# Kernel optimization log

Hardware: AMD Instinct MI355X
Metric: run time of the kernel (lower is better)

## Reference

```python
import jax, jax.numpy as jnp
import numpy as np

EMBED_DIM = 1024
NUM_HEADS = 16
HEAD_DIM = EMBED_DIM // NUM_HEADS


def setup_inputs() -> dict:
    key = jax.random.key(0)
    ks = jax.random.split(key, 11)
    N, S, D = 2, 2048, EMBED_DIM
    scale = 1.0 / np.sqrt(D)
    inp = {
        "query": jax.random.normal(ks[0], (N, S, D), jnp.float32),
        "key": jax.random.normal(ks[1], (N, S, D), jnp.float32),
        "value": jax.random.normal(ks[2], (N, S, D), jnp.float32),
        # Dense layer params (kernel [D_in, D_out], bias [D_out])
        "Wq": jax.random.normal(ks[3], (D, D), jnp.float32) * scale,
        "bq": jnp.zeros((D,), jnp.float32),
        "Wk": jax.random.normal(ks[4], (D, D), jnp.float32) * scale,
        "bk": jnp.zeros((D,), jnp.float32),
        "Wv": jax.random.normal(ks[5], (D, D), jnp.float32) * scale,
        "bv": jnp.zeros((D,), jnp.float32),
        "Wp": jax.random.normal(ks[6], (D, D), jnp.float32) * scale,
        "bp": jnp.zeros((D,), jnp.float32),
    }
    return inp


def reference(query, key, value, Wq, bq, Wk, bk, Wv, bv, Wp, bp):
    N, S, D = query.shape
    H, Hd = NUM_HEADS, D // NUM_HEADS
    # Linear projections, then split heads: [N, H, S, Hd]
    def split_heads(x):
        return x.reshape(N, S, H, Hd).transpose(0, 2, 1, 3)
    q = split_heads(query @ Wq + bq)
    k = split_heads(key @ Wk + bk)
    v = split_heads(value @ Wv + bv)
    # Scaled dot-product attention; materializes [N, H, S, S] scores
    e = jnp.einsum("bhsd,bhtd->bhst", q, k) / jnp.sqrt(jnp.asarray(Hd, jnp.float32))
    a = jax.nn.softmax(e, axis=-1)
    # Dropout is identity in inference mode (keras Dropout default)
    out = jnp.einsum("bhst,bhtd->bhsd", a, v)
    out = out.transpose(0, 2, 1, 3).reshape(N, S, D)
    return out @ Wp + bp
```

## Files before the change

kernel.cpp:

```cpp
#include <hip/hip_runtime.h>
#include <cstdint>
#include <cstddef>

typedef _Float16 f16;
typedef f16 f16x2 __attribute__((ext_vector_type(2)));
typedef f16 f16x8 __attribute__((ext_vector_type(8)));
typedef __fp16 hf16x2 __attribute__((ext_vector_type(2)));
typedef float f32x4 __attribute__((ext_vector_type(4)));
typedef float f32x16 __attribute__((ext_vector_type(16)));
typedef unsigned int u32;

#define S_LEN 2048
#define DIM 1024
#define NBATCH 2
#define NHEAD 16
#define HDIM 64
#define M_TOT (NBATCH * S_LEN)

#define QSCALE 0.18033688011112042f

#define OFF_XQ 0ull
#define OFF_XK (OFF_XQ + (size_t)M_TOT * DIM * 2)
#define OFF_XV (OFF_XK + (size_t)M_TOT * DIM * 2)
#define OFF_WT (OFF_XV + (size_t)M_TOT * DIM * 2)
#define OFF_Q  (OFF_WT + 4ull * DIM * DIM * 2)
#define OFF_K  (OFF_Q + (size_t)M_TOT * DIM * 2)
#define OFF_VT (OFF_K + (size_t)M_TOT * DIM * 2)
#define OFF_AO (OFF_VT + (size_t)M_TOT * DIM * 2)

typedef const __attribute__((address_space(1))) void GVp;
typedef __attribute__((address_space(3))) void LVp;
__device__ __forceinline__ void gload16(const void* g, void* l) {
  __builtin_amdgcn_global_load_lds((GVp*)g, (LVp*)l, 16, 0, 0);
}

__device__ __forceinline__ float fast_exp2(float x) {
  float r;
  asm("v_exp_f32 %0, %1" : "=v"(r) : "v"(x));
  return r;
}

__global__ __launch_bounds__(256) void cast_x_kernel(
    const float* __restrict__ q, const float* __restrict__ k, const float* __restrict__ v,
    f16* __restrict__ oq, f16* __restrict__ ok, f16* __restrict__ ov) {
  const float* src = blockIdx.y == 0 ? q : blockIdx.y == 1 ? k : v;
  f16* dst = blockIdx.y == 0 ? oq : blockIdx.y == 1 ? ok : ov;
  size_t i = ((size_t)blockIdx.x * 256 + threadIdx.x) * 8;
  float4 a = *(const float4*)(src + i);
  float4 b = *(const float4*)(src + i + 4);
  f16x8 o;
  o[0] = (f16)a.x; o[1] = (f16)a.y; o[2] = (f16)a.z; o[3] = (f16)a.w;
  o[4] = (f16)b.x; o[5] = (f16)b.y; o[6] = (f16)b.z; o[7] = (f16)b.w;
  *(f16x8*)(dst + i) = o;
}

__global__ __launch_bounds__(256) void transpose_w_kernel(
    const float* __restrict__ Wq, const float* __restrict__ Wk,
    const float* __restrict__ Wv, const float* __restrict__ Wp,
    f16* __restrict__ out) {
  const float* W = blockIdx.z == 0 ? Wq : blockIdx.z == 1 ? Wk : blockIdx.z == 2 ? Wv : Wp;
  f16* Wt = out + (size_t)blockIdx.z * DIM * DIM;
  __shared__ f16 tile[64][72];
  const int kt = blockIdx.x * 64, nt = blockIdx.y * 64;
  const int t = threadIdx.x, r = t >> 2, c0 = (t & 3) * 16;
#pragma unroll
  for (int i = 0; i < 16; i += 4) {
    float4 vv = *(const float4*)(W + (size_t)(kt + r) * DIM + nt + c0 + i);
    tile[r][c0 + i + 0] = (f16)vv.x; tile[r][c0 + i + 1] = (f16)vv.y;
    tile[r][c0 + i + 2] = (f16)vv.z; tile[r][c0 + i + 3] = (f16)vv.w;
  }
  __syncthreads();
  f16x8 o0, o1;
#pragma unroll
  for (int i = 0; i < 8; ++i) { o0[i] = tile[c0 + i][r]; o1[i] = tile[c0 + 8 + i][r]; }
  *(f16x8*)(Wt + (size_t)(nt + r) * DIM + kt + c0) = o0;
  *(f16x8*)(Wt + (size_t)(nt + r) * DIM + kt + c0 + 8) = o1;
}

__device__ __forceinline__ void gemm_core(const f16* __restrict__ A, const f16* __restrict__ B,
                                          char* lds, f32x4 acc[4][4]) {
  const int tid = threadIdx.x;
  const int wid = tid >> 6, lane = tid & 63;
  const int l15 = lane & 15, l4 = lane >> 4;
  const int wm = (wid >> 1) * 64, wn = (wid & 1) * 64;
  const int srow = tid >> 2;
  const int scol = (tid & 3) * 8;
  const f16* gA = A + (size_t)srow * DIM + scol;
  const f16* gB = B + (size_t)srow * DIM + scol;
  const int ldst = wid * 1024;

  gload16(gA,            lds + ldst);
  gload16(gA + 64 * DIM, lds + 4096 + ldst);
  gload16(gB,            lds + 8192 + ldst);
  gload16(gB + 64 * DIM, lds + 12288 + ldst);
  __syncthreads();

  for (int kt = 0; kt < DIM / 32; ++kt) {
    char* cur = lds + (kt & 1) * 16384;
    if (kt + 1 < DIM / 32) {
      char* nxt = lds + ((kt + 1) & 1) * 16384;
      const f16* ga = gA + (kt + 1) * 32;
      const f16* gb = gB + (kt + 1) * 32;
      gload16(ga,            nxt + ldst);
      gload16(ga + 64 * DIM, nxt + 4096 + ldst);
      gload16(gb,            nxt + 8192 + ldst);
      gload16(gb + 64 * DIM, nxt + 12288 + ldst);
    }
    f16x8 af[4], bf[4];
#pragma unroll
    for (int mt = 0; mt < 4; ++mt)
      af[mt] = *(const f16x8*)(cur + (wm + mt * 16 + l15) * 64 + l4 * 16);
#pragma unroll
    for (int nt = 0; nt < 4; ++nt)
      bf[nt] = *(const f16x8*)(cur + 8192 + (wn + nt * 16 + l15) * 64 + l4 * 16);
#pragma unroll
    for (int mt = 0; mt < 4; ++mt)
#pragma unroll
      for (int nt = 0; nt < 4; ++nt)
        acc[mt][nt] = __builtin_amdgcn_mfma_f32_16x16x32_f16(af[mt], bf[nt], acc[mt][nt], 0, 0, 0);
    __syncthreads();
  }
}


__global__ __launch_bounds__(256) void proj_kernel(
    const f16* __restrict__ Xq, const f16* __restrict__ Xk, const f16* __restrict__ Xv,
    const f16* __restrict__ Wt,
    const float* __restrict__ bq, const float* __restrict__ bk, const float* __restrict__ bv,
    f16* __restrict__ Q, f16* __restrict__ Kh, f16* __restrict__ Vt) {
  __shared__ __align__(16) char lds[32768];
  const int m0 = blockIdx.x * 128, n0 = blockIdx.y * 128;
  const int z = blockIdx.z;
  const f16* X = z == 0 ? Xq : z == 1 ? Xk : Xv;
  const f16* W = Wt + (size_t)z * DIM * DIM;
  const float* bias = z == 0 ? bq : z == 1 ? bk : bv;
  f32x4 acc[4][4] = {};
  gemm_core(X + (size_t)m0 * DIM, W + (size_t)n0 * DIM, lds, acc);

  const int tid = threadIdx.x, wid = tid >> 6, lane = tid & 63;
  const int l15 = lane & 15, l4 = lane >> 4;
  const int wm = (wid >> 1) * 64, wn = (wid & 1) * 64;
#pragma unroll
  for (int nt = 0; nt < 4; ++nt) {
    const int col = n0 + wn + nt * 16 + l15;
    const float bb = bias[col];
    const int hh = col >> 6, d = col & 63;
#pragma unroll
    for (int mt = 0; mt < 4; ++mt)
#pragma unroll
      for (int j = 0; j < 4; ++j) {
        const int row = m0 + wm + mt * 16 + l4 * 4 + j;
        const float v = acc[mt][nt][j] + bb;
        const int n = row >> 11, s = row & (S_LEN - 1);
        const size_t panel = (size_t)(n * NHEAD + hh);
        if (z == 0) {
          const size_t a = panel * (S_LEN * HDIM) + (size_t)(s >> 5) * 2048 +
                           (d >> 4) * 512 + ((d >> 3) & 1) * 256 + (s & 31) * 8 + (d & 7);
          Q[a] = (f16)(v * QSCALE);
        } else if (z == 1) {
          const size_t a = panel * (S_LEN * HDIM) + (size_t)(s >> 5) * 2048 +
                           (d >> 4) * 512 + ((d >> 3) & 1) * 256 + (s & 31) * 8 + (d & 7);
          Kh[a] = (f16)v;
        } else {
          const size_t a = panel * (S_LEN * HDIM) + (size_t)(s >> 6) * 4096 +
                           (d >> 5) * 2048 + ((s >> 4) & 3) * 512 + ((s >> 3) & 1) * 256 +
                           (d & 31) * 8 + (s & 7);
          Vt[a] = (f16)v;
        }
      }
  }
}

__global__ __launch_bounds__(256) void outproj_kernel(
    const f16* __restrict__ A, const f16* __restrict__ Wt,
    const float* __restrict__ bias, float* __restrict__ Out) {
  __shared__ __align__(16) char lds[32768];
  const int m0 = blockIdx.x * 128, n0 = blockIdx.y * 128;
  f32x4 acc[4][4] = {};
  gemm_core(A + (size_t)m0 * DIM, Wt + (size_t)n0 * DIM, lds, acc);

  const int tid = threadIdx.x, wid = tid >> 6, lane = tid & 63;
  const int l15 = lane & 15, l4 = lane >> 4;
  const int wm = (wid >> 1) * 64, wn = (wid & 1) * 64;
#pragma unroll
  for (int nt = 0; nt < 4; ++nt) {
    const int col = n0 + wn + nt * 16 + l15;
    const float bb = bias[col];
#pragma unroll
    for (int mt = 0; mt < 4; ++mt)
#pragma unroll
      for (int j = 0; j < 4; ++j) {
        const int row = m0 + wm + mt * 16 + l4 * 4 + j;
        Out[(size_t)row * DIM + col] = acc[mt][nt][j] + bb;
      }
  }
}

__global__ __launch_bounds__(256, 1) void attn_kernel(
    const f16* __restrict__ Q, const f16* __restrict__ K,
    const f16* __restrict__ Vt, f16* __restrict__ AO) {
  const int qt = blockIdx.x, h = blockIdx.y, b = blockIdx.z;
  const int lane = threadIdx.x & 63, wid = threadIdx.x >> 6;
  const int l31 = lane & 31, hi = lane >> 5;

  const int q0 = qt * 128 + wid * 32;
  const size_t panel = (size_t)(b * NHEAD + h) * (S_LEN * HDIM);
  const f16* Qp = Q + panel + (size_t)(q0 >> 5) * 2048;
  const f16* Kp = K + panel;
  const f16* Vp = Vt + panel;

  f16x8 qf[4];
#pragma unroll
  for (int sk = 0; sk < 4; ++sk)
    qf[sk] = *(const f16x8*)(Qp + sk * 512 + hi * 256 + l31 * 8);

  f32x16 accO[2] = {};
  float lacc0 = 0.f, lacc1 = 0.f, lacc2 = 0.f, lacc3 = 0.f;

  auto LOADK = [&](int it, f16x8 (&kf)[2][4]) {
#pragma unroll
    for (int tt = 0; tt < 2; ++tt)
#pragma unroll
      for (int sk = 0; sk < 4; ++sk)
        kf[tt][sk] = *(const f16x8*)(Kp + (size_t)(it * 2 + tt) * 2048 + sk * 512 + hi * 256 + l31 * 8);
  };
  auto LOADV = [&](int it, f16x8 (&vf)[2][4]) {
#pragma unroll
    for (int dt = 0; dt < 2; ++dt)
#pragma unroll
      for (int s = 0; s < 4; ++s)
        vf[dt][s] = *(const f16x8*)(Vp + (size_t)it * 4096 + dt * 2048 + s * 512 + hi * 256 + l31 * 8);
  };
  auto QK = [&](const f16x8 (&kf)[2][4], f32x16 (&st)[2]) {
    __builtin_amdgcn_s_setprio(1);
#pragma unroll
    for (int tt = 0; tt < 2; ++tt) {
      st[tt] = (f32x16)(0.f);
#pragma unroll
      for (int sk = 0; sk < 4; ++sk)
        st[tt] = __builtin_amdgcn_mfma_f32_32x32x16_f16(kf[tt][sk], qf[sk], st[tt], 0, 0, 0);
    }
    __builtin_amdgcn_s_setprio(0);
  };

  auto PHASE = [&](f32x16 (&st)[2], const f16x8 (&vf)[2][4]) {
    u32 pk[2][8];
#pragma unroll
    for (int tt = 0; tt < 2; ++tt)
#pragma unroll
      for (int j = 0; j < 8; ++j) {
        const float p0 = fast_exp2(st[tt][2 * j]);
        const float p1 = fast_exp2(st[tt][2 * j + 1]);
        const float ps = p0 + p1;
        if (((tt * 8 + j) & 3) == 0) lacc0 += ps;
        else if (((tt * 8 + j) & 3) == 1) lacc1 += ps;
        else if (((tt * 8 + j) & 3) == 2) lacc2 += ps;
        else lacc3 += ps;
        union { hf16x2 h; u32 w; } cv;
        cv.h = __builtin_amdgcn_cvt_pkrtz(p0, p1);
        pk[tt][j] = cv.w;
      }

    __builtin_amdgcn_s_setprio(1);
#pragma unroll
    for (int s = 0; s < 4; ++s) {
      const int tt = s >> 1, sl = s & 1;
      u32 w0 = pk[tt][4 * sl + 0], w2 = pk[tt][4 * sl + 2];
      u32 w1 = pk[tt][4 * sl + 1], w3 = pk[tt][4 * sl + 3];
      asm("v_permlane32_swap_b32 %0, %1" : "+v"(w0), "+v"(w2));
      asm("v_permlane32_swap_b32 %0, %1" : "+v"(w1), "+v"(w3));
      union { u32 w[4]; f16x8 v; } pf;
      pf.w[0] = w0; pf.w[1] = w1; pf.w[2] = w2; pf.w[3] = w3;
      accO[0] = __builtin_amdgcn_mfma_f32_32x32x16_f16(vf[0][s], pf.v, accO[0], 0, 0, 0);
      accO[1] = __builtin_amdgcn_mfma_f32_32x32x16_f16(vf[1][s], pf.v, accO[1], 0, 0, 0);
    }
    __builtin_amdgcn_s_setprio(0);
  };

  f16x8 kfA[2][4], kfB[2][4], vfA[2][4], vfB[2][4];
  f32x16 st[2];
  LOADK(0, kfA); LOADV(0, vfA);
  LOADK(1, kfB); LOADV(1, vfB);
  QK(kfA, st);

  for (int it = 0; it < S_LEN / 64 - 2; it += 2) {
    PHASE(st, vfA);
    LOADV(it + 2, vfA);
    QK(kfB, st);
    LOADK(it + 2, kfA);
    PHASE(st, vfB);
    LOADV(it + 3, vfB);
    QK(kfA, st);
    LOADK(it + 3, kfB);
  }
  PHASE(st, vfA);
  QK(kfB, st);
  PHASE(st, vfB);

  const float l_loc = (lacc0 + lacc1) + (lacc2 + lacc3);
  const float l_all = l_loc + __shfl_xor(l_loc, 32);
  const float inv = 1.f / l_all;
  f16* aop = AO + ((size_t)(b * S_LEN + q0 + l31)) * DIM + h * HDIM;
#pragma unroll
  for (int dt = 0; dt < 2; ++dt)
#pragma unroll
    for (int j = 0; j < 8; ++j) {
      union { f16x2 h; u32 w; } cv;
      cv.h[0] = (f16)(accO[dt][2 * j] * inv);
      cv.h[1] = (f16)(accO[dt][2 * j + 1] * inv);
      const int d = ((2 * j) & 3) + 8 * ((2 * j) >> 2) + 4 * hi + dt * 32;
      *(f16x2*)(aop + d) = cv.h;
    }
}

extern "C" void kernel_launch(void* const* d_in, const int* in_sizes, int n_in,
                              void* d_out, int out_size, void* d_ws, size_t ws_size,
                              hipStream_t stream) {
  (void)in_sizes; (void)n_in; (void)out_size; (void)ws_size;
  const float* q  = (const float*)d_in[0];
  const float* k  = (const float*)d_in[1];
  const float* v  = (const float*)d_in[2];
  const float* Wq = (const float*)d_in[3];
  const float* bq = (const float*)d_in[4];
  const float* Wk = (const float*)d_in[5];
  const float* bk = (const float*)d_in[6];
  const float* Wv = (const float*)d_in[7];
  const float* bv = (const float*)d_in[8];
  const float* Wp = (const float*)d_in[9];
  const float* bp = (const float*)d_in[10];

  char* ws = (char*)d_ws;
  f16* Xq  = (f16*)(ws + OFF_XQ);
  f16* Xk  = (f16*)(ws + OFF_XK);
  f16* Xv  = (f16*)(ws + OFF_XV);
  f16* Wt  = (f16*)(ws + OFF_WT);
  f16* Qs  = (f16*)(ws + OFF_Q);
  f16* Kh  = (f16*)(ws + OFF_K);
  f16* Vts = (f16*)(ws + OFF_VT);
  f16* AO  = (f16*)(ws + OFF_AO);

  cast_x_kernel<<<dim3(2048, 3, 1), 256, 0, stream>>>(q, k, v, Xq, Xk, Xv);
  transpose_w_kernel<<<dim3(16, 16, 4), 256, 0, stream>>>(Wq, Wk, Wv, Wp, Wt);
  proj_kernel<<<dim3(32, 8, 3), 256, 0, stream>>>(Xq, Xk, Xv, Wt, bq, bk, bv, Qs, Kh, Vts);
  attn_kernel<<<dim3(16, 16, 2), 256, 0, stream>>>(Qs, Kh, Vts, AO);
  outproj_kernel<<<dim3(32, 8, 1), 256, 0, stream>>>(AO, Wt + 3ull * DIM * DIM, bp, (float*)d_out);
}
```

Before: 136.3 us.

## Stage K/V tiles through double-buffered LDS shared across waves in attention

Replaces the per-wave direct global loads of K and V fragments, which had each of the four waves load the same tiles separately, with cooperative block-wide loads into a double-buffered LDS staging area. Each wave then reads its fragments from LDS. The aim is to cut redundant global/L2 traffic by a factor of four and to free the registers that held two sets of prefetched fragments, so launch bounds is raised to allow two blocks per CU. In exchange it adds a __syncthreads per iteration and LDS read latency, and it drops the explicit two-deep register prefetch interleaving.

```diff
diff --git a/kernel.cpp b/kernel.cpp
--- a/kernel.cpp
+++ b/kernel.cpp
@@ -196,18 +196,21 @@
   }
 }
 
-__global__ __launch_bounds__(256, 1) void attn_kernel(
+__global__ __launch_bounds__(256, 2) void attn_kernel(
     const f16* __restrict__ Q, const f16* __restrict__ K,
     const f16* __restrict__ Vt, f16* __restrict__ AO) {
   const int qt = blockIdx.x, h = blockIdx.y, b = blockIdx.z;
-  const int lane = threadIdx.x & 63, wid = threadIdx.x >> 6;
+  const int tid = threadIdx.x;
+  const int lane = tid & 63, wid = tid >> 6;
   const int l31 = lane & 31, hi = lane >> 5;
+
+  __shared__ __align__(16) char kv_lds[2][16384];
 
   const int q0 = qt * 128 + wid * 32;
   const size_t panel = (size_t)(b * NHEAD + h) * (S_LEN * HDIM);
   const f16* Qp = Q + panel + (size_t)(q0 >> 5) * 2048;
-  const f16* Kp = K + panel;
-  const f16* Vp = Vt + panel;
+  const char* KpB = (const char*)(K + panel);
+  const char* VpB = (const char*)(Vt + panel);
 
   f16x8 qf[4];
 #pragma unroll
@@ -217,21 +220,24 @@
   f32x16 accO[2] = {};
   float lacc0 = 0.f, lacc1 = 0.f, lacc2 = 0.f, lacc3 = 0.f;
 
-  auto LOADK = [&](int it, f16x8 (&kf)[2][4]) {
+  auto STAGE = [&](int it, int buf) {
+    const char* gK = KpB + (size_t)it * 8192 + tid * 16;
+    const char* gV = VpB + (size_t)it * 8192 + tid * 16;
+    char* lb = kv_lds[buf] + (tid >> 6) * 1024;
+    gload16(gK,        lb);
+    gload16(gK + 4096, lb + 4096);
+    gload16(gV,        lb + 8192);
+    gload16(gV + 4096, lb + 12288);
+  };
+
+  auto QK = [&](int buf, f32x16 (&st)[2]) {
+    const char* lk = kv_lds[buf];
+    f16x8 kf[2][4];
 #pragma unroll
     for (int tt = 0; tt < 2; ++tt)
 #pragma unroll
       for (int sk = 0; sk < 4; ++sk)
-        kf[tt][sk] = *(const f16x8*)(Kp + (size_t)(it * 2 + tt) * 2048 + sk * 512 + hi * 256 + l31 * 8);
-  };
-  auto LOADV = [&](int it, f16x8 (&vf)[2][4]) {
-#pragma unroll
-    for (int dt = 0; dt < 2; ++dt)
-#pragma unroll
-      for (int s = 0; s < 4; ++s)
-        vf[dt][s] = *(const f16x8*)(Vp + (size_t)it * 4096 + dt * 2048 + s * 512 + hi * 256 + l31 * 8);
-  };
-  auto QK = [&](const f16x8 (&kf)[2][4], f32x16 (&st)[2]) {
+        kf[tt][sk] = *(const f16x8*)(lk + tt * 4096 + sk * 1024 + lane * 16);
     __builtin_amdgcn_s_setprio(1);
 #pragma unroll
     for (int tt = 0; tt < 2; ++tt) {
@@ -243,7 +249,15 @@
     __builtin_amdgcn_s_setprio(0);
   };
 
-  auto PHASE = [&](f32x16 (&st)[2], const f16x8 (&vf)[2][4]) {
+  auto PHASE = [&](f32x16 (&st)[2], int buf) {
+    const char* lv = kv_lds[buf] + 8192;
+    f16x8 vf[2][4];
+#pragma unroll
+    for (int dt = 0; dt < 2; ++dt)
+#pragma unroll
+      for (int s = 0; s < 4; ++s)
+        vf[dt][s] = *(const f16x8*)(lv + dt * 4096 + s * 1024 + lane * 16);
+
     u32 pk[2][8];
 #pragma unroll
     for (int tt = 0; tt < 2; ++tt)
@@ -277,25 +291,18 @@
     __builtin_amdgcn_s_setprio(0);
   };
 
-  f16x8 kfA[2][4], kfB[2][4], vfA[2][4], vfB[2][4];
+  const int NIT = S_LEN / 64;
+  STAGE(0, 0);
+  __syncthreads();
+
   f32x16 st[2];
-  LOADK(0, kfA); LOADV(0, vfA);
-  LOADK(1, kfB); LOADV(1, vfB);
-  QK(kfA, st);
-
-  for (int it = 0; it < S_LEN / 64 - 2; it += 2) {
-    PHASE(st, vfA);
-    LOADV(it + 2, vfA);
-    QK(kfB, st);
-    LOADK(it + 2, kfA);
-    PHASE(st, vfB);
-    LOADV(it + 3, vfB);
-    QK(kfA, st);
-    LOADK(it + 3, kfB);
-  }
-  PHASE(st, vfA);
-  QK(kfB, st);
-  PHASE(st, vfB);
+  for (int it = 0; it < NIT; ++it) {
+    const int buf = it & 1;
+    if (it + 1 < NIT) STAGE(it + 1, buf ^ 1);
+    QK(buf, st);
+    PHASE(st, buf);
+    __syncthreads();
+  }
 
   const float l_loc = (lacc0 + lacc1) + (lacc2 + lacc3);
   const float l_all = l_loc + __shfl_xor(l_loc, 32);
```

Measured after the change: 131.8 us. -3.3%, faster.

## Fuse input fp32 cast into projection GEMM and split attention KV range across waves

Applied to the files above, without the earlier changes.

Drops the separate cast kernel: the projection GEMM now streams fp32 activations straight into LDS and converts them to fp16 while building fragments, which removes one full write-and-reread of the three input tensors. The attention kernel is restructured so each 128-thread block handles 32 queries with two waves, each wave covering half the key sequence. The two partial results are then merged through shared memory. This gives four times as many, smaller blocks, trading higher occupancy and parallelism for extra LDS traffic, a larger A-tile in LDS, and a combine step. The split merge skips max rescaling, which is only valid if the softmax does not subtract a running max.

```diff
diff --git a/kernel.cpp b/kernel.cpp
--- a/kernel.cpp
+++ b/kernel.cpp
@@ -19,10 +19,7 @@
 
 #define QSCALE 0.18033688011112042f
 
-#define OFF_XQ 0ull
-#define OFF_XK (OFF_XQ + (size_t)M_TOT * DIM * 2)
-#define OFF_XV (OFF_XK + (size_t)M_TOT * DIM * 2)
-#define OFF_WT (OFF_XV + (size_t)M_TOT * DIM * 2)
+#define OFF_WT 0ull
 #define OFF_Q  (OFF_WT + 4ull * DIM * DIM * 2)
 #define OFF_K  (OFF_Q + (size_t)M_TOT * DIM * 2)
 #define OFF_VT (OFF_K + (size_t)M_TOT * DIM * 2)
@@ -38,20 +35,6 @@
   float r;
   asm("v_exp_f32 %0, %1" : "=v"(r) : "v"(x));
   return r;
-}
-
-__global__ __launch_bounds__(256) void cast_x_kernel(
-    const float* __restrict__ q, const float* __restrict__ k, const float* __restrict__ v,
-    f16* __restrict__ oq, f16* __restrict__ ok, f16* __restrict__ ov) {
-  const float* src = blockIdx.y == 0 ? q : blockIdx.y == 1 ? k : v;
-  f16* dst = blockIdx.y == 0 ? oq : blockIdx.y == 1 ? ok : ov;
-  size_t i = ((size_t)blockIdx.x * 256 + threadIdx.x) * 8;
-  float4 a = *(const float4*)(src + i);
-  float4 b = *(const float4*)(src + i + 4);
-  f16x8 o;
-  o[0] = (f16)a.x; o[1] = (f16)a.y; o[2] = (f16)a.z; o[3] = (f16)a.w;
-  o[4] = (f16)b.x; o[5] = (f16)b.y; o[6] = (f16)b.z; o[7] = (f16)b.w;
-  *(f16x8*)(dst + i) = o;
 }
 
 __global__ __launch_bounds__(256) void transpose_w_kernel(
@@ -75,6 +58,57 @@
   for (int i = 0; i < 8; ++i) { o0[i] = tile[c0 + i][r]; o1[i] = tile[c0 + 8 + i][r]; }
   *(f16x8*)(Wt + (size_t)(nt + r) * DIM + kt + c0) = o0;
   *(f16x8*)(Wt + (size_t)(nt + r) * DIM + kt + c0 + 8) = o1;
+}
+
+__device__ __forceinline__ void gemm_core_af32(const float* __restrict__ A, const f16* __restrict__ B,
+                                               char* lds, f32x4 acc[4][4]) {
+  const int tid = threadIdx.x;
+  const int wid = tid >> 6, lane = tid & 63;
+  const int l15 = lane & 15, l4 = lane >> 4;
+  const int wm = (wid >> 1) * 64, wn = (wid & 1) * 64;
+  const float* gA = A + (size_t)(tid >> 3) * DIM + (tid & 7) * 4;
+  const f16* gB = B + (size_t)(tid >> 2) * DIM + (tid & 3) * 8;
+  const int ldst = wid * 1024;
+
+  auto stage = [&](int kt, char* buf) {
+    const float* ga = gA + kt * 32;
+    const f16* gb = gB + kt * 32;
+#pragma unroll
+    for (int i = 0; i < 4; ++i)
+      gload16(ga + (size_t)i * 32 * DIM, buf + i * 4096 + ldst);
+    gload16(gb,            buf + 16384 + ldst);
+    gload16(gb + 64 * DIM, buf + 20480 + ldst);
+  };
+
+  stage(0, lds);
+  __syncthreads();
+
+  for (int kt = 0; kt < DIM / 32; ++kt) {
+    char* cur = lds + (kt & 1) * 24576;
+    if (kt + 1 < DIM / 32) stage(kt + 1, lds + ((kt + 1) & 1) * 24576);
+    f16x8 af[4], bf[4];
+#pragma unroll
+    for (int mt = 0; mt < 4; ++mt) {
+      const char* ap = cur + ((wm >> 5) + (mt >> 1)) * 4096 + (((mt & 1) * 16 + l15) * 128) + l4 * 32;
+      f32x4 lo = *(const f32x4*)ap;
+      f32x4 hi = *(const f32x4*)(ap + 16);
+      union { hf16x2 h[4]; f16x8 v; } cv;
+      cv.h[0] = __builtin_amdgcn_cvt_pkrtz(lo[0], lo[1]);
+      cv.h[1] = __builtin_amdgcn_cvt_pkrtz(lo[2], lo[3]);
+      cv.h[2] = __builtin_amdgcn_cvt_pkrtz(hi[0], hi[1]);
+      cv.h[3] = __builtin_amdgcn_cvt_pkrtz(hi[2], hi[3]);
+      af[mt] = cv.v;
+    }
+#pragma unroll
+    for (int nt = 0; nt < 4; ++nt)
+      bf[nt] = *(const f16x8*)(cur + 16384 + (wn + nt * 16 + l15) * 64 + l4 * 16);
+#pragma unroll
+    for (int mt = 0; mt < 4; ++mt)
+#pragma unroll
+      for (int nt = 0; nt < 4; ++nt)
+        acc[mt][nt] = __builtin_amdgcn_mfma_f32_16x16x32_f16(af[mt], bf[nt], acc[mt][nt], 0, 0, 0);
+    __syncthreads();
+  }
 }
 
 __device__ __forceinline__ void gemm_core(const f16* __restrict__ A, const f16* __restrict__ B,
@@ -124,18 +158,18 @@
 
 
 __global__ __launch_bounds__(256) void proj_kernel(
-    const f16* __restrict__ Xq, const f16* __restrict__ Xk, const f16* __restrict__ Xv,
+    const float* __restrict__ Xq, const float* __restrict__ Xk, const float* __restrict__ Xv,
     const f16* __restrict__ Wt,
     const float* __restrict__ bq, const float* __restrict__ bk, const float* __restrict__ bv,
     f16* __restrict__ Q, f16* __restrict__ Kh, f16* __restrict__ Vt) {
-  __shared__ __align__(16) char lds[32768];
+  __shared__ __align__(16) char lds[49152];
   const int m0 = blockIdx.x * 128, n0 = blockIdx.y * 128;
   const int z = blockIdx.z;
-  const f16* X = z == 0 ? Xq : z == 1 ? Xk : Xv;
+  const float* X = z == 0 ? Xq : z == 1 ? Xk : Xv;
   const f16* W = Wt + (size_t)z * DIM * DIM;
   const float* bias = z == 0 ? bq : z == 1 ? bk : bv;
   f32x4 acc[4][4] = {};
-  gemm_core(X + (size_t)m0 * DIM, W + (size_t)n0 * DIM, lds, acc);
+  gemm_core_af32(X + (size_t)m0 * DIM, W + (size_t)n0 * DIM, lds, acc);
 
   const int tid = threadIdx.x, wid = tid >> 6, lane = tid & 63;
   const int l15 = lane & 15, l4 = lane >> 4;
@@ -196,14 +230,17 @@
   }
 }
 
-__global__ __launch_bounds__(256, 1) void attn_kernel(
+__global__ __launch_bounds__(128) void attn_kernel(
     const f16* __restrict__ Q, const f16* __restrict__ K,
     const f16* __restrict__ Vt, f16* __restrict__ AO) {
   const int qt = blockIdx.x, h = blockIdx.y, b = blockIdx.z;
-  const int lane = threadIdx.x & 63, wid = threadIdx.x >> 6;
+  const int tid = threadIdx.x;
+  const int lane = tid & 63, half = tid >> 6;
   const int l31 = lane & 31, hi = lane >> 5;
 
-  const int q0 = qt * 128 + wid * 32;
+  __shared__ float comb[2048 + 64];
+
+  const int q0 = qt * 32;
   const size_t panel = (size_t)(b * NHEAD + h) * (S_LEN * HDIM);
   const f16* Qp = Q + panel + (size_t)(q0 >> 5) * 2048;
   const f16* Kp = K + panel;
@@ -277,13 +314,15 @@
     __builtin_amdgcn_s_setprio(0);
   };
 
+  const int i0 = half * 16;
+
   f16x8 kfA[2][4], kfB[2][4], vfA[2][4], vfB[2][4];
   f32x16 st[2];
-  LOADK(0, kfA); LOADV(0, vfA);
-  LOADK(1, kfB); LOADV(1, vfB);
+  LOADK(i0, kfA); LOADV(i0, vfA);
+  LOADK(i0 + 1, kfB); LOADV(i0 + 1, vfB);
   QK(kfA, st);
 
-  for (int it = 0; it < S_LEN / 64 - 2; it += 2) {
+  for (int it = i0; it < i0 + 14; it += 2) {
     PHASE(st, vfA);
     LOADV(it + 2, vfA);
     QK(kfB, st);
@@ -298,19 +337,36 @@
   PHASE(st, vfB);
 
   const float l_loc = (lacc0 + lacc1) + (lacc2 + lacc3);
-  const float l_all = l_loc + __shfl_xor(l_loc, 32);
-  const float inv = 1.f / l_all;
-  f16* aop = AO + ((size_t)(b * S_LEN + q0 + l31)) * DIM + h * HDIM;
-#pragma unroll
-  for (int dt = 0; dt < 2; ++dt)
-#pragma unroll
-    for (int j = 0; j < 8; ++j) {
-      union { f16x2 h; u32 w; } cv;
-      cv.h[0] = (f16)(accO[dt][2 * j] * inv);
-      cv.h[1] = (f16)(accO[dt][2 * j + 1] * inv);
-      const int d = ((2 * j) & 3) + 8 * ((2 * j) >> 2) + 4 * hi + dt * 32;
-      *(f16x2*)(aop + d) = cv.h;
-    }
+  if (half == 1) {
+#pragma unroll
+    for (int dt = 0; dt < 2; ++dt)
+#pragma unroll
+      for (int j = 0; j < 16; ++j)
+        comb[(dt * 16 + j) * 64 + lane] = accO[dt][j];
+    comb[2048 + lane] = l_loc;
+  }
+  __syncthreads();
+  if (half == 0) {
+#pragma unroll
+    for (int dt = 0; dt < 2; ++dt)
+#pragma unroll
+      for (int j = 0; j < 16; ++j)
+        accO[dt][j] += comb[(dt * 16 + j) * 64 + lane];
+    const float l2 = l_loc + comb[2048 + lane];
+    const float l_all = l2 + __shfl_xor(l2, 32);
+    const float inv = 1.f / l_all;
+    f16* aop = AO + ((size_t)(b * S_LEN + q0 + l31)) * DIM + h * HDIM;
+#pragma unroll
+    for (int dt = 0; dt < 2; ++dt)
+#pragma unroll
+      for (int j = 0; j < 8; ++j) {
+        union { f16x2 h; u32 w; } cv;
+        cv.h[0] = (f16)(accO[dt][2 * j] * inv);
+        cv.h[1] = (f16)(accO[dt][2 * j + 1] * inv);
+        const int d = ((2 * j) & 3) + 8 * ((2 * j) >> 2) + 4 * hi + dt * 32;
+        *(f16x2*)(aop + d) = cv.h;
+      }
+  }
 }
 
 extern "C" void kernel_launch(void* const* d_in, const int* in_sizes, int n_in,
@@ -330,18 +386,14 @@
   const float* bp = (const float*)d_in[10];
 
   char* ws = (char*)d_ws;
-  f16* Xq  = (f16*)(ws + OFF_XQ);
-  f16* Xk  = (f16*)(ws + OFF_XK);
-  f16* Xv  = (f16*)(ws + OFF_XV);
   f16* Wt  = (f16*)(ws + OFF_WT);
   f16* Qs  = (f16*)(ws + OFF_Q);
   f16* Kh  = (f16*)(ws + OFF_K);
   f16* Vts = (f16*)(ws + OFF_VT);
   f16* AO  = (f16*)(ws + OFF_AO);
 
-  cast_x_kernel<<<dim3(2048, 3, 1), 256, 0, stream>>>(q, k, v, Xq, Xk, Xv);
   transpose_w_kernel<<<dim3(16, 16, 4), 256, 0, stream>>>(Wq, Wk, Wv, Wp, Wt);
-  proj_kernel<<<dim3(32, 8, 3), 256, 0, stream>>>(Xq, Xk, Xv, Wt, bq, bk, bv, Qs, Kh, Vts);
-  attn_kernel<<<dim3(16, 16, 2), 256, 0, stream>>>(Qs, Kh, Vts, AO);
+  proj_kernel<<<dim3(32, 8, 3), 256, 0, stream>>>(q, k, v, Wt, bq, bk, bv, Qs, Kh, Vts);
+  attn_kernel<<<dim3(64, 16, 2), 128, 0, stream>>>(Qs, Kh, Vts, AO);
   outproj_kernel<<<dim3(32, 8, 1), 256, 0, stream>>>(AO, Wt + 3ull * DIM * DIM, bp, (float*)d_out);
 }
```

Measured after the change: 135.7 us. No clear change (-0.5%).

## Split attention KV range across two waves and swizzle out-projection LDS

Applied to the files above, without the earlier changes.

The attention kernel now uses 128-thread blocks with one 32-row query tile each. The two waves split the key/value sequence in half and merge their partial outputs and row sums through shared memory. This creates four times as many blocks for better occupancy and latency hiding, at the cost of an LDS reduction. It appears to rely on softmax without a running max, as the original did. Separately, the out-projection GEMM gets an XOR-swizzled LDS layout to reduce bank conflicts.

```diff
diff --git a/kernel.cpp b/kernel.cpp
--- a/kernel.cpp
+++ b/kernel.cpp
@@ -113,6 +113,52 @@
 #pragma unroll
     for (int nt = 0; nt < 4; ++nt)
       bf[nt] = *(const f16x8*)(cur + 8192 + (wn + nt * 16 + l15) * 64 + l4 * 16);
+#pragma unroll
+    for (int mt = 0; mt < 4; ++mt)
+#pragma unroll
+      for (int nt = 0; nt < 4; ++nt)
+        acc[mt][nt] = __builtin_amdgcn_mfma_f32_16x16x32_f16(af[mt], bf[nt], acc[mt][nt], 0, 0, 0);
+    __syncthreads();
+  }
+}
+
+__device__ __forceinline__ void gemm_core_sw(const f16* __restrict__ A, const f16* __restrict__ B,
+                                             char* lds, f32x4 acc[4][4]) {
+  const int tid = threadIdx.x;
+  const int wid = tid >> 6, lane = tid & 63;
+  const int l15 = lane & 15, l4 = lane >> 4;
+  const int wm = (wid >> 1) * 64, wn = (wid & 1) * 64;
+  const int rr = tid >> 2, cc = tid & 3;
+  const int ccs = cc ^ ((rr >> 1) & 3);
+  const f16* gA = A + (size_t)rr * DIM + ccs * 8;
+  const f16* gB = B + (size_t)rr * DIM + ccs * 8;
+  const int ldst = wid * 1024;
+
+  gload16(gA,            lds + ldst);
+  gload16(gA + 64 * DIM, lds + 4096 + ldst);
+  gload16(gB,            lds + 8192 + ldst);
+  gload16(gB + 64 * DIM, lds + 12288 + ldst);
+  __syncthreads();
+
+  const int sw = (l15 >> 1) & 3;
+  for (int kt = 0; kt < DIM / 32; ++kt) {
+    char* cur = lds + (kt & 1) * 16384;
+    if (kt + 1 < DIM / 32) {
+      char* nxt = lds + ((kt + 1) & 1) * 16384;
+      const f16* ga = gA + (kt + 1) * 32;
+      const f16* gb = gB + (kt + 1) * 32;
+      gload16(ga,            nxt + ldst);
+      gload16(ga + 64 * DIM, nxt + 4096 + ldst);
+      gload16(gb,            nxt + 8192 + ldst);
+      gload16(gb + 64 * DIM, nxt + 12288 + ldst);
+    }
+    f16x8 af[4], bf[4];
+#pragma unroll
+    for (int mt = 0; mt < 4; ++mt)
+      af[mt] = *(const f16x8*)(cur + (wm + mt * 16 + l15) * 64 + (l4 ^ sw) * 16);
+#pragma unroll
+    for (int nt = 0; nt < 4; ++nt)
+      bf[nt] = *(const f16x8*)(cur + 8192 + (wn + nt * 16 + l15) * 64 + (l4 ^ sw) * 16);
 #pragma unroll
     for (int mt = 0; mt < 4; ++mt)
 #pragma unroll
@@ -177,7 +223,7 @@
   __shared__ __align__(16) char lds[32768];
   const int m0 = blockIdx.x * 128, n0 = blockIdx.y * 128;
   f32x4 acc[4][4] = {};
-  gemm_core(A + (size_t)m0 * DIM, Wt + (size_t)n0 * DIM, lds, acc);
+  gemm_core_sw(A + (size_t)m0 * DIM, Wt + (size_t)n0 * DIM, lds, acc);
 
   const int tid = threadIdx.x, wid = tid >> 6, lane = tid & 63;
   const int l15 = lane & 15, l4 = lane >> 4;
@@ -196,14 +242,17 @@
   }
 }
 
-__global__ __launch_bounds__(256, 1) void attn_kernel(
+__global__ __launch_bounds__(128) void attn_kernel(
     const f16* __restrict__ Q, const f16* __restrict__ K,
     const f16* __restrict__ Vt, f16* __restrict__ AO) {
   const int qt = blockIdx.x, h = blockIdx.y, b = blockIdx.z;
-  const int lane = threadIdx.x & 63, wid = threadIdx.x >> 6;
+  const int tid = threadIdx.x;
+  const int lane = tid & 63, half = tid >> 6;
   const int l31 = lane & 31, hi = lane >> 5;
 
-  const int q0 = qt * 128 + wid * 32;
+  __shared__ float comb[2048 + 64];
+
+  const int q0 = qt * 32;
   const size_t panel = (size_t)(b * NHEAD + h) * (S_LEN * HDIM);
   const f16* Qp = Q + panel + (size_t)(q0 >> 5) * 2048;
   const f16* Kp = K + panel;
@@ -277,13 +326,15 @@
     __builtin_amdgcn_s_setprio(0);
   };
 
+  const int i0 = half * 16;
+
   f16x8 kfA[2][4], kfB[2][4], vfA[2][4], vfB[2][4];
   f32x16 st[2];
-  LOADK(0, kfA); LOADV(0, vfA);
-  LOADK(1, kfB); LOADV(1, vfB);
+  LOADK(i0, kfA); LOADV(i0, vfA);
+  LOADK(i0 + 1, kfB); LOADV(i0 + 1, vfB);
   QK(kfA, st);
 
-  for (int it = 0; it < S_LEN / 64 - 2; it += 2) {
+  for (int it = i0; it < i0 + 14; it += 2) {
     PHASE(st, vfA);
     LOADV(it + 2, vfA);
     QK(kfB, st);
@@ -298,19 +349,36 @@
   PHASE(st, vfB);
 
   const float l_loc = (lacc0 + lacc1) + (lacc2 + lacc3);
-  const float l_all = l_loc + __shfl_xor(l_loc, 32);
-  const float inv = 1.f / l_all;
-  f16* aop = AO + ((size_t)(b * S_LEN + q0 + l31)) * DIM + h * HDIM;
-#pragma unroll
-  for (int dt = 0; dt < 2; ++dt)
-#pragma unroll
-    for (int j = 0; j < 8; ++j) {
-      union { f16x2 h; u32 w; } cv;
-      cv.h[0] = (f16)(accO[dt][2 * j] * inv);
-      cv.h[1] = (f16)(accO[dt][2 * j + 1] * inv);
-      const int d = ((2 * j) & 3) + 8 * ((2 * j) >> 2) + 4 * hi + dt * 32;
-      *(f16x2*)(aop + d) = cv.h;
-    }
+  if (half == 1) {
+#pragma unroll
+    for (int dt = 0; dt < 2; ++dt)
+#pragma unroll
+      for (int j = 0; j < 16; ++j)
+        comb[(dt * 16 + j) * 64 + lane] = accO[dt][j];
+    comb[2048 + lane] = l_loc;
+  }
+  __syncthreads();
+  if (half == 0) {
+#pragma unroll
+    for (int dt = 0; dt < 2; ++dt)
+#pragma unroll
+      for (int j = 0; j < 16; ++j)
+        accO[dt][j] += comb[(dt * 16 + j) * 64 + lane];
+    const float l2 = l_loc + comb[2048 + lane];
+    const float l_all = l2 + __shfl_xor(l2, 32);
+    const float inv = 1.f / l_all;
+    f16* aop = AO + ((size_t)(b * S_LEN + q0 + l31)) * DIM + h * HDIM;
+#pragma unroll
+    for (int dt = 0; dt < 2; ++dt)
+#pragma unroll
+      for (int j = 0; j < 8; ++j) {
+        union { f16x2 h; u32 w; } cv;
+        cv.h[0] = (f16)(accO[dt][2 * j] * inv);
+        cv.h[1] = (f16)(accO[dt][2 * j + 1] * inv);
+        const int d = ((2 * j) & 3) + 8 * ((2 * j) >> 2) + 4 * hi + dt * 32;
+        *(f16x2*)(aop + d) = cv.h;
+      }
+  }
 }
 
 extern "C" void kernel_launch(void* const* d_in, const int* in_sizes, int n_in,
@@ -342,6 +410,6 @@
   cast_x_kernel<<<dim3(2048, 3, 1), 256, 0, stream>>>(q, k, v, Xq, Xk, Xv);
   transpose_w_kernel<<<dim3(16, 16, 4), 256, 0, stream>>>(Wq, Wk, Wv, Wp, Wt);
   proj_kernel<<<dim3(32, 8, 3), 256, 0, stream>>>(Xq, Xk, Xv, Wt, bq, bk, bv, Qs, Kh, Vts);
-  attn_kernel<<<dim3(16, 16, 2), 256, 0, stream>>>(Qs, Kh, Vts, AO);
+  attn_kernel<<<dim3(64, 16, 2), 128, 0, stream>>>(Qs, Kh, Vts, AO);
   outproj_kernel<<<dim3(32, 8, 1), 256, 0, stream>>>(AO, Wt + 3ull * DIM * DIM, bp, (float*)d_out);
 }
```

After: 140.8 us. +3.3%, slower.
